# Optimization experiments

Measured on AMD Instinct MI355X. Metric: run time of the kernel, lower is better.

Reference implementation:

```python
import jax, jax.numpy as jnp
import numpy as np

B, T, D, NH, L, E, K = 2, 1024, 512, 8, 4, 8, 2
H = D * 4
HD = D // NH
EPS = 1e-5
THETA = 10000.0
MOE_LAYERS = (0, 2)   # layer_idx % moe_freq == 0
DENSE_LAYERS = (1, 3)


def setup_inputs() -> dict:
    key = jax.random.key(0)
    ks = jax.random.split(key, 12)
    s = 0.02
    return {
        "x": jax.random.normal(ks[0], (B, T, D), jnp.float32),
        "qkv_w": jax.random.normal(ks[1], (L, 3 * D, D), jnp.float32) * s,
        "out_w": jax.random.normal(ks[2], (L, D, D), jnp.float32) * s,
        "norm1_w": jnp.ones((L, D), jnp.float32),
        "norm2_w": jnp.ones((L, D), jnp.float32),
        "router_w": jax.random.normal(ks[3], (2, E, D), jnp.float32) * s,
        "moe_w1": jax.random.normal(ks[4], (2, E, H, D), jnp.float32) * s,
        "moe_w2": jax.random.normal(ks[5], (2, E, D, H), jnp.float32) * s,
        "moe_w3": jax.random.normal(ks[6], (2, E, H, D), jnp.float32) * s,
        "f_w1": jax.random.normal(ks[7], (2, H, D), jnp.float32) * s,
        "f_w2": jax.random.normal(ks[8], (2, D, H), jnp.float32) * s,
        "f_w3": jax.random.normal(ks[9], (2, H, D), jnp.float32) * s,
        "norm_f": jnp.ones((D,), jnp.float32),
    }


def rmsnorm(x, w):
    return w * x * jax.lax.rsqrt(jnp.mean(x * x, axis=-1, keepdims=True) + EPS)


def rope_tables():
    inv_freq = 1.0 / (THETA ** (jnp.arange(0, HD, 2, dtype=jnp.float32) / HD))  # [HD/2]
    t = jnp.arange(T, dtype=jnp.float32)
    freqs = t[:, None] * inv_freq[None, :]  # [T, HD/2]
    return jnp.cos(freqs), jnp.sin(freqs)


def apply_rope(x, cos, sin):  # x: [B, NH, T, HD]
    x1, x2 = jnp.split(x, 2, axis=-1)
    return jnp.concatenate([x1 * cos - x2 * sin, x1 * sin + x2 * cos], axis=-1)


def attention(x, qkv_w, out_w, cos, sin, causal):
    qkv = x @ qkv_w.T  # [B, T, 3D]
    q, k, v = jnp.split(qkv, 3, axis=-1)
    sh = lambda a: a.reshape(B, T, NH, HD).transpose(0, 2, 1, 3)  # [B, NH, T, HD]
    q, k, v = sh(q), sh(k), sh(v)
    q = apply_rope(q, cos, sin)
    k = apply_rope(k, cos, sin)
    scores = jnp.einsum('bhqd,bhkd->bhqk', q, k) / np.sqrt(HD).astype(np.float32)
    scores = jnp.where(causal, scores, jnp.finfo(scores.dtype).min)
    attn = jax.nn.softmax(scores, axis=-1)
    out = jnp.einsum('bhqk,bhkd->bhqd', attn, v)
    out = out.transpose(0, 2, 1, 3).reshape(B, T, D)
    return out @ out_w.T


def swiglu(x, w1, w2, w3):
    return (jax.nn.silu(x @ w1.T) * (x @ w3.T)) @ w2.T


def moe(x, rw, w1, w2, w3):  # x: [N, D]
    n = x.shape[0]
    logits = x @ rw.T                              # [N, E]
    top_v, top_i = jax.lax.top_k(logits, K)        # [N, K]
    wts = jax.nn.softmax(top_v, axis=-1)           # [N, K]
    # combine[t, e] = sum_i wts[t, i] * 1[top_i[t, i] == e]
    combine = jnp.zeros((n, E), x.dtype).at[jnp.arange(n)[:, None], top_i].add(wts)
    gate = jax.nn.silu(jnp.einsum('nd,ehd->neh', x, w1))
    up = jnp.einsum('nd,ehd->neh', x, w3)
    expert_out = jnp.einsum('neh,edh->ned', gate * up, w2)  # [N, E, D]
    return jnp.einsum('ne,ned->nd', combine, expert_out)


def reference(x, qkv_w, out_w, norm1_w, norm2_w, router_w, moe_w1, moe_w2,
              moe_w3, f_w1, f_w2, f_w3, norm_f):
    cos, sin = rope_tables()
    causal = jnp.tril(jnp.ones((T, T), bool))
    h = x
    for l in range(L):
        h = h + attention(rmsnorm(h, norm1_w[l]), qkv_w[l], out_w[l], cos, sin, causal)
        hn = rmsnorm(h, norm2_w[l])
        if l in MOE_LAYERS:
            m = MOE_LAYERS.index(l)
            ff = moe(hn.reshape(-1, D), router_w[m], moe_w1[m], moe_w2[m], moe_w3[m]).reshape(B, T, D)
        else:
            m = DENSE_LAYERS.index(l)
            ff = swiglu(hn, f_w1[m], f_w2[m], f_w3[m])
        h = h + ff
    return rmsnorm(h, norm_f)
```

## Files before the change

kernel.cpp:

```cpp
#include <hip/hip_runtime.h>
#include <hip/hip_bf16.h>
#include <math.h>

#define Bc 2
#define Tc 1024
#define Dc 512
#define NHc 8
#define Lc 4
#define Ec 8
#define Kc 2
#define Hc 2048
#define HDc 64
#define Nc (Bc * Tc)
#define NKc (Nc * Kc)

typedef __bf16 bf16x8 __attribute__((ext_vector_type(8)));
typedef float  f32x4  __attribute__((ext_vector_type(4)));
typedef unsigned short ushort8v __attribute__((ext_vector_type(8)));
typedef unsigned short ushort4v __attribute__((ext_vector_type(4)));

__device__ inline unsigned short f2bf(float f) {
    union { float f; unsigned u; } v; v.f = f;
    unsigned r = v.u + 0x7FFFu + ((v.u >> 16) & 1u);
    return (unsigned short)(r >> 16);
}
__device__ inline float bf2f(unsigned short b) {
    union { unsigned u; float f; } v; v.u = ((unsigned)b) << 16;
    return v.f;
}
__device__ inline void splitbf(float a, unsigned short& hi, unsigned short& lo) {
    unsigned short h = f2bf(a);
    hi = h;
    lo = f2bf(a - bf2f(h));
}

__global__ __launch_bounds__(256) void split_w_kernel(
    const float* __restrict__ w, unsigned short* __restrict__ hi,
    unsigned short* __restrict__ lo, int n4)
{
    int i = blockIdx.x * 256 + threadIdx.x;
    if (i >= n4) return;
    float4 v = ((const float4*)w)[i];
    ushort4v h, l;
    unsigned short a, b;
    splitbf(v.x, a, b); h[0] = a; l[0] = b;
    splitbf(v.y, a, b); h[1] = a; l[1] = b;
    splitbf(v.z, a, b); h[2] = a; l[2] = b;
    splitbf(v.w, a, b); h[3] = a; l[3] = b;
    ((ushort4v*)hi)[i] = h;
    ((ushort4v*)lo)[i] = l;
}

__global__ __launch_bounds__(256) void rmsnorm_split_kernel(
    const float* __restrict__ x, const float* __restrict__ w,
    float* __restrict__ y, unsigned short* __restrict__ yh,
    unsigned short* __restrict__ yl)
{
    int row = blockIdx.x;
    const float* xr = x + (size_t)row * Dc;
    __shared__ float red[256];
    int tid = threadIdx.x;
    float ss = 0.0f;
    for (int d = tid; d < Dc; d += 256) { float v = xr[d]; ss += v * v; }
    red[tid] = ss; __syncthreads();
    for (int s = 128; s > 0; s >>= 1) {
        if (tid < s) red[tid] += red[tid + s];
        __syncthreads();
    }
    float inv = rsqrtf(red[0] / (float)Dc + 1e-5f);
    for (int d = tid; d < Dc; d += 256) {
        float v = w[d] * xr[d] * inv;
        size_t idx = (size_t)row * Dc + d;
        y[idx] = v;
        unsigned short h, l;
        splitbf(v, h, l);
        yh[idx] = h; yl[idx] = l;
    }
}

__global__ __launch_bounds__(256) void rmsnorm_kernel(
    const float* __restrict__ x, const float* __restrict__ w,
    float* __restrict__ y)
{
    int row = blockIdx.x;
    const float* xr = x + (size_t)row * Dc;
    __shared__ float red[256];
    int tid = threadIdx.x;
    float ss = 0.0f;
    for (int d = tid; d < Dc; d += 256) { float v = xr[d]; ss += v * v; }
    red[tid] = ss; __syncthreads();
    for (int s = 128; s > 0; s >>= 1) {
        if (tid < s) red[tid] += red[tid + s];
        __syncthreads();
    }
    float inv = rsqrtf(red[0] / (float)Dc + 1e-5f);
    for (int d = tid; d < Dc; d += 256)
        y[(size_t)row * Dc + d] = w[d] * xr[d] * inv;
}

template<int MODE, int TM, int TN, int KSPLIT>
__global__ __launch_bounds__(256) void gemm3p(
    const unsigned short* __restrict__ Ahi, const unsigned short* __restrict__ Alo,
    const unsigned short* __restrict__ Whibase, const unsigned short* __restrict__ Wlobase,
    float* __restrict__ C, int M, int N, int K,
    const int* __restrict__ tok, const float* __restrict__ twt,
    const int* __restrict__ counts, const int* __restrict__ offsets,
    size_t wstride)
{
    constexpr int PAD = 40;
    constexpr int PA  = TM / 64;
    constexpr int PB  = TN / 64;
    constexpr int FM  = TM / 32;
    constexpr int FN  = TN / 32;

    int zz = blockIdx.z;
    int e  = (MODE == 5) ? zz / KSPLIT : 0;
    int kz = (MODE == 5) ? zz % KSPLIT : zz;
    int count = M, offs = 0;
    if (MODE == 5) {
        count = counts[e];
        offs  = offsets[e];
        if ((int)(blockIdx.y * TM) >= count) return;
    }
    const unsigned short* Whi = Whibase + (size_t)e * wstride;
    const unsigned short* Wlo = Wlobase + (size_t)e * wstride;

    int Ksub = K / KSPLIT;
    int kbeg = kz * Ksub;

    __shared__ __align__(16) unsigned short Ah[TM][PAD];
    __shared__ __align__(16) unsigned short Al[TM][PAD];
    __shared__ __align__(16) unsigned short Bh[TN][PAD];
    __shared__ __align__(16) unsigned short Bl[TN][PAD];

    int tid = threadIdx.x;
    int m0 = blockIdx.y * TM, n0 = blockIdx.x * TN;
    int srow = tid >> 2;
    int scol = (tid & 3) * 8;

    int wave = tid >> 6, lane = tid & 63;
    int wm = wave >> 1, wn = wave & 1;
    int quad = lane >> 4, l16 = lane & 15;

    f32x4 acc[FM][FN];
#pragma unroll
    for (int mi = 0; mi < FM; ++mi)
#pragma unroll
        for (int ni = 0; ni < FN; ++ni)
            acc[mi][ni] = (f32x4){0.f, 0.f, 0.f, 0.f};

    size_t arow[PA];
#pragma unroll
    for (int p = 0; p < PA; ++p) {
        int row = p * 64 + srow;
        if (MODE == 5) {
            int rr = m0 + row; if (rr >= count) rr = 0;
            arow[p] = (size_t)(offs + rr) * K;
        } else {
            arow[p] = (size_t)(m0 + row) * K;
        }
    }
    size_t brow[PB];
#pragma unroll
    for (int p = 0; p < PB; ++p)
        brow[p] = (size_t)(n0 + p * 64 + srow) * K;

#define G3_LOAD(AH, AL, BH, BL, KN)                                       \
    {                                                                     \
        _Pragma("unroll")                                                 \
        for (int p = 0; p < PA; ++p) {                                    \
            AH[p] = *(const ushort8v*)(Ahi + arow[p] + (KN) + scol);      \
            AL[p] = *(const ushort8v*)(Alo + arow[p] + (KN) + scol);      \
        }                                                                 \
        _Pragma("unroll")                                                 \
        for (int p = 0; p < PB; ++p) {                                    \
            BH[p] = *(const ushort8v*)(Whi + brow[p] + (KN) + scol);      \
            BL[p] = *(const ushort8v*)(Wlo + brow[p] + (KN) + scol);      \
        }                                                                 \
    }

#define G3_STORE(AH, AL, BH, BL)                                          \
    {                                                                     \
        _Pragma("unroll")                                                 \
        for (int p = 0; p < PA; ++p) {                                    \
            *(ushort8v*)&Ah[p * 64 + srow][scol] = AH[p];                 \
            *(ushort8v*)&Al[p * 64 + srow][scol] = AL[p];                 \
        }                                                                 \
        _Pragma("unroll")                                                 \
        for (int p = 0; p < PB; ++p) {                                    \
            *(ushort8v*)&Bh[p * 64 + srow][scol] = BH[p];                 \
            *(ushort8v*)&Bl[p * 64 + srow][scol] = BL[p];                 \
        }                                                                 \
    }

#define G3_COMPUTE()                                                      \
    {                                                                     \
        bf16x8 ah[FM], al[FM], bh[FN], bl[FN];                            \
        _Pragma("unroll")                                                 \
        for (int mi = 0; mi < FM; ++mi) {                                 \
            ah[mi] = *(const bf16x8*)&Ah[wm * (TM / 2) + mi * 16 + l16][quad * 8]; \
            al[mi] = *(const bf16x8*)&Al[wm * (TM / 2) + mi * 16 + l16][quad * 8]; \
        }                                                                 \
        _Pragma("unroll")                                                 \
        for (int ni = 0; ni < FN; ++ni) {                                 \
            bh[ni] = *(const bf16x8*)&Bh[wn * (TN / 2) + ni * 16 + l16][quad * 8]; \
            bl[ni] = *(const bf16x8*)&Bl[wn * (TN / 2) + ni * 16 + l16][quad * 8]; \
        }                                                                 \
        _Pragma("unroll")                                                 \
        for (int mi = 0; mi < FM; ++mi)                                   \
            _Pragma("unroll")                                             \
            for (int ni = 0; ni < FN; ++ni) {                             \
                acc[mi][ni] = __builtin_amdgcn_mfma_f32_16x16x32_bf16(    \
                    ah[mi], bh[ni], acc[mi][ni], 0, 0, 0);                \
                acc[mi][ni] = __builtin_amdgcn_mfma_f32_16x16x32_bf16(    \
                    al[mi], bh[ni], acc[mi][ni], 0, 0, 0);                \
                acc[mi][ni] = __builtin_amdgcn_mfma_f32_16x16x32_bf16(    \
                    ah[mi], bl[ni], acc[mi][ni], 0, 0, 0);                \
            }                                                             \
    }

    ushort8v a0h[PA], a0l[PA], b0h[PB], b0l[PB];
    ushort8v a1h[PA], a1l[PA], b1h[PB], b1l[PB];
    G3_LOAD(a0h, a0l, b0h, b0l, kbeg)
    G3_LOAD(a1h, a1l, b1h, b1l, kbeg + 32)

    for (int k0 = kbeg; k0 < kbeg + Ksub; k0 += 64) {
        G3_STORE(a0h, a0l, b0h, b0l)
        __syncthreads();
        if (k0 + 64 < kbeg + Ksub) G3_LOAD(a0h, a0l, b0h, b0l, k0 + 64)
        G3_COMPUTE()
        __syncthreads();
        G3_STORE(a1h, a1l, b1h, b1l)
        __syncthreads();
        if (k0 + 96 < kbeg + Ksub) G3_LOAD(a1h, a1l, b1h, b1l, k0 + 96)
        G3_COMPUTE()
        __syncthreads();
    }
#undef G3_LOAD
#undef G3_STORE
#undef G3_COMPUTE

#pragma unroll
    for (int mi = 0; mi < FM; ++mi) {
#pragma unroll
        for (int ni = 0; ni < FN; ++ni) {
            int col = n0 + wn * (TN / 2) + ni * 16 + l16;
#pragma unroll
            for (int r = 0; r < 4; ++r) {
                int row = wm * (TM / 2) + mi * 16 + quad * 4 + r;
                float v = acc[mi][ni][r];
                if (MODE == 0) {
                    C[(size_t)(m0 + row) * N + col] = v;
                } else if (MODE == 1) {
                    C[(size_t)(m0 + row) * N + col] += v;
                } else if (MODE == 2) {
                    atomicAdd(&C[(size_t)(m0 + row) * N + col], v);
                } else {
                    int rr = m0 + row;
                    if (rr < count) {
                        int dest = tok[offs + rr];
                        float w = twt[offs + rr];
                        atomicAdd(&C[(size_t)dest * N + col], w * v);
                    }
                }
            }
        }
    }
}

template<bool GATHER>
__global__ __launch_bounds__(512) void ffn_fusedp(
    const unsigned short* __restrict__ Ahi, const unsigned short* __restrict__ Alo,
    const unsigned short* __restrict__ W1hibase, const unsigned short* __restrict__ W1lobase,
    const unsigned short* __restrict__ W3hibase, const unsigned short* __restrict__ W3lobase,
    unsigned short* __restrict__ Thi, unsigned short* __restrict__ Tlo,
    int M, int N, int K,
    const int* __restrict__ tok, const int* __restrict__ counts,
    const int* __restrict__ offsets, size_t wstride)
{
    constexpr int TM = 128, TN = 128, PAD = 40;
    constexpr int FM = 4, FN = 2;

    int e = GATHER ? blockIdx.z : 0;
    int count = M, offs = 0;
    if (GATHER) {
        count = counts[e];
        offs  = offsets[e];
        if ((int)(blockIdx.y * TM) >= count) return;
    }
    const unsigned short* W1hi = W1hibase + (size_t)e * wstride;
    const unsigned short* W1lo = W1lobase + (size_t)e * wstride;
    const unsigned short* W3hi = W3hibase + (size_t)e * wstride;
    const unsigned short* W3lo = W3lobase + (size_t)e * wstride;

    __shared__ __align__(16) unsigned short Ah[TM][PAD];
    __shared__ __align__(16) unsigned short Al[TM][PAD];
    __shared__ __align__(16) unsigned short B1h[TN][PAD];
    __shared__ __align__(16) unsigned short B1l[TN][PAD];
    __shared__ __align__(16) unsigned short B3h[TN][PAD];
    __shared__ __align__(16) unsigned short B3l[TN][PAD];
    __shared__ int sTok[TM];

    int tid = threadIdx.x;
    int m0 = blockIdx.y * TM, n0 = blockIdx.x * TN;

    if (GATHER) {
        if (tid < TM) {
            int r = m0 + tid;
            sTok[tid] = (r < count) ? tok[offs + r] : tok[offs];
        }
        __syncthreads();
    }

    int srow = tid >> 2;
    int scol = (tid & 3) * 8;
    int wave = tid >> 6, lane = tid & 63;
    int wm = wave >> 2, wn = wave & 3;
    int quad = lane >> 4, l16 = lane & 15;

    f32x4 accg[FM][FN], accu[FM][FN];
#pragma unroll
    for (int mi = 0; mi < FM; ++mi)
#pragma unroll
        for (int ni = 0; ni < FN; ++ni) {
            accg[mi][ni] = (f32x4){0.f, 0.f, 0.f, 0.f};
            accu[mi][ni] = (f32x4){0.f, 0.f, 0.f, 0.f};
        }

    size_t arow;
    if (GATHER) arow = (size_t)sTok[srow] * K;
    else        arow = (size_t)(m0 + srow) * K;
    size_t brow = (size_t)(n0 + srow) * K;

    ushort8v pah, pal, p1h, p1l, p3h, p3l;
    pah = *(const ushort8v*)(Ahi + arow + scol);
    pal = *(const ushort8v*)(Alo + arow + scol);
    p1h = *(const ushort8v*)(W1hi + brow + scol);
    p1l = *(const ushort8v*)(W1lo + brow + scol);
    p3h = *(const ushort8v*)(W3hi + brow + scol);
    p3l = *(const ushort8v*)(W3lo + brow + scol);

    for (int k0 = 0; k0 < K; k0 += 32) {
        *(ushort8v*)&Ah[srow][scol]  = pah;
        *(ushort8v*)&Al[srow][scol]  = pal;
        *(ushort8v*)&B1h[srow][scol] = p1h;
        *(ushort8v*)&B1l[srow][scol] = p1l;
        *(ushort8v*)&B3h[srow][scol] = p3h;
        *(ushort8v*)&B3l[srow][scol] = p3l;
        __syncthreads();
        if (k0 + 32 < K) {
            int kn = k0 + 32;
            pah = *(const ushort8v*)(Ahi + arow + kn + scol);
            pal = *(const ushort8v*)(Alo + arow + kn + scol);
            p1h = *(const ushort8v*)(W1hi + brow + kn + scol);
            p1l = *(const ushort8v*)(W1lo + brow + kn + scol);
            p3h = *(const ushort8v*)(W3hi + brow + kn + scol);
            p3l = *(const ushort8v*)(W3lo + brow + kn + scol);
        }

        bf16x8 ah[FM], al[FM];
#pragma unroll
        for (int mi = 0; mi < FM; ++mi) {
            ah[mi] = *(const bf16x8*)&Ah[wm * 64 + mi * 16 + l16][quad * 8];
            al[mi] = *(const bf16x8*)&Al[wm * 64 + mi * 16 + l16][quad * 8];
        }
        {
            bf16x8 bh[FN], bl[FN];
#pragma unroll
            for (int ni = 0; ni < FN; ++ni) {
                bh[ni] = *(const bf16x8*)&B1h[wn * 32 + ni * 16 + l16][quad * 8];
                bl[ni] = *(const bf16x8*)&B1l[wn * 32 + ni * 16 + l16][quad * 8];
            }
#pragma unroll
            for (int mi = 0; mi < FM; ++mi)
#pragma unroll
                for (int ni = 0; ni < FN; ++ni) {
                    accg[mi][ni] = __builtin_amdgcn_mfma_f32_16x16x32_bf16(
                        ah[mi], bh[ni], accg[mi][ni], 0, 0, 0);
                    accg[mi][ni] = __builtin_amdgcn_mfma_f32_16x16x32_bf16(
                        al[mi], bh[ni], accg[mi][ni], 0, 0, 0);
                    accg[mi][ni] = __builtin_amdgcn_mfma_f32_16x16x32_bf16(
                        ah[mi], bl[ni], accg[mi][ni], 0, 0, 0);
                }
        }
        {
            bf16x8 bh[FN], bl[FN];
#pragma unroll
            for (int ni = 0; ni < FN; ++ni) {
                bh[ni] = *(const bf16x8*)&B3h[wn * 32 + ni * 16 + l16][quad * 8];
                bl[ni] = *(const bf16x8*)&B3l[wn * 32 + ni * 16 + l16][quad * 8];
            }
#pragma unroll
            for (int mi = 0; mi < FM; ++mi)
#pragma unroll
                for (int ni = 0; ni < FN; ++ni) {
                    accu[mi][ni] = __builtin_amdgcn_mfma_f32_16x16x32_bf16(
                        ah[mi], bh[ni], accu[mi][ni], 0, 0, 0);
                    accu[mi][ni] = __builtin_amdgcn_mfma_f32_16x16x32_bf16(
                        al[mi], bh[ni], accu[mi][ni], 0, 0, 0);
                    accu[mi][ni] = __builtin_amdgcn_mfma_f32_16x16x32_bf16(
                        ah[mi], bl[ni], accu[mi][ni], 0, 0, 0);
                }
        }
        __syncthreads();
    }

#pragma unroll
    for (int mi = 0; mi < FM; ++mi) {
#pragma unroll
        for (int ni = 0; ni < FN; ++ni) {
            int col = n0 + wn * 32 + ni * 16 + l16;
#pragma unroll
            for (int r = 0; r < 4; ++r) {
                int row = wm * 64 + mi * 16 + quad * 4 + r;
                float g = accg[mi][ni][r];
                float u = accu[mi][ni][r];
                float t = (g / (1.0f + expf(-g))) * u;
                unsigned short th, tl;
                splitbf(t, th, tl);
                if (GATHER) {
                    int rr = m0 + row;
                    if (rr < count) {
                        size_t idx = (size_t)(offs + rr) * N + col;
                        Thi[idx] = th; Tlo[idx] = tl;
                    }
                } else {
                    size_t idx = (size_t)(m0 + row) * N + col;
                    Thi[idx] = th; Tlo[idx] = tl;
                }
            }
        }
    }
}

__global__ __launch_bounds__(256) void rope_kernel(float* __restrict__ qkv)
{
    const int HD2 = HDc / 2;
    int idx = blockIdx.x * blockDim.x + threadIdx.x;
    int total = Nc * NHc * HD2;
    if (idx >= total) return;
    int i = idx % HD2;
    int hh = (idx / HD2) % NHc;
    int n = idx / (HD2 * NHc);
    int t = n % Tc;
    float invf = expf(-(2.0f * (float)i / (float)HDc) * logf(10000.0f));
    float f = (float)t * invf;
    float c = cosf(f), s = sinf(f);
    size_t base = (size_t)n * (3 * Dc) + (size_t)hh * HDc;
    float* qp = qkv + base;
    float* kp = qkv + base + Dc;
    float q1 = qp[i], q2 = qp[i + HD2];
    qp[i]       = q1 * c - q2 * s;
    qp[i + HD2] = q1 * s + q2 * c;
    float k1 = kp[i], k2 = kp[i + HD2];
    kp[i]       = k1 * c - k2 * s;
    kp[i + HD2] = k1 * s + k2 * c;
}

__global__ __launch_bounds__(256) void attn_mfma(
    const float* __restrict__ qkv, unsigned short* __restrict__ outh,
    unsigned short* __restrict__ outl)
{
    constexpr int PAD = 72;
    __shared__ __align__(16) unsigned short Qh[64][PAD];
    __shared__ __align__(16) unsigned short Ql[64][PAD];
    __shared__ __align__(16) unsigned short Kh[64][PAD];
    __shared__ __align__(16) unsigned short Kl[64][PAD];
    __shared__ __align__(16) unsigned short Vth[64][PAD];
    __shared__ __align__(16) unsigned short Vtl[64][PAD];

    int qb = blockIdx.x, bh = blockIdx.y;
    int b = bh >> 3, hh = bh & 7;
    const int D3 = 3 * Dc;
    const float* base = qkv + (size_t)b * Tc * D3 + (size_t)hh * HDc;

    int tid = threadIdx.x;
    int wave = tid >> 6, lane = tid & 63;
    int quad = lane >> 4, l16 = lane & 15;

    int srow = tid >> 2;
    int scb  = (tid & 3) * 16;
    int vhd  = lane;
    int vkb  = wave * 16;

    {
        const float* qp = base + (size_t)(qb * 64 + srow) * D3 + scb;
        float4 q0 = *(const float4*)(qp);
        float4 q1 = *(const float4*)(qp + 4);
        float4 q2 = *(const float4*)(qp + 8);
        float4 q3 = *(const float4*)(qp + 12);
        const float sc = 0.125f;
        q0.x *= sc; q0.y *= sc; q0.z *= sc; q0.w *= sc;
        q1.x *= sc; q1.y *= sc; q1.z *= sc; q1.w *= sc;
        q2.x *= sc; q2.y *= sc; q2.z *= sc; q2.w *= sc;
        q3.x *= sc; q3.y *= sc; q3.z *= sc; q3.w *= sc;
        unsigned short h, l;
        ushort8v hv, lv;
        splitbf(q0.x, h, l); hv[0] = h; lv[0] = l;
        splitbf(q0.y, h, l); hv[1] = h; lv[1] = l;
        splitbf(q0.z, h, l); hv[2] = h; lv[2] = l;
        splitbf(q0.w, h, l); hv[3] = h; lv[3] = l;
        splitbf(q1.x, h, l); hv[4] = h; lv[4] = l;
        splitbf(q1.y, h, l); hv[5] = h; lv[5] = l;
        splitbf(q1.z, h, l); hv[6] = h; lv[6] = l;
        splitbf(q1.w, h, l); hv[7] = h; lv[7] = l;
        *(ushort8v*)&Qh[srow][scb]     = hv;
        *(ushort8v*)&Ql[srow][scb]     = lv;
        splitbf(q2.x, h, l); hv[0] = h; lv[0] = l;
        splitbf(q2.y, h, l); hv[1] = h; lv[1] = l;
        splitbf(q2.z, h, l); hv[2] = h; lv[2] = l;
        splitbf(q2.w, h, l); hv[3] = h; lv[3] = l;
        splitbf(q3.x, h, l); hv[4] = h; lv[4] = l;
        splitbf(q3.y, h, l); hv[5] = h; lv[5] = l;
        splitbf(q3.z, h, l); hv[6] = h; lv[6] = l;
        splitbf(q3.w, h, l); hv[7] = h; lv[7] = l;
        *(ushort8v*)&Qh[srow][scb + 8] = hv;
        *(ushort8v*)&Ql[srow][scb + 8] = lv;
    }
    __syncthreads();
    bf16x8 qah[2], qal[2];
#pragma unroll
    for (int ks = 0; ks < 2; ++ks) {
        qah[ks] = *(const bf16x8*)&Qh[wave * 16 + l16][ks * 32 + quad * 8];
        qal[ks] = *(const bf16x8*)&Ql[wave * 16 + l16][ks * 32 + quad * 8];
    }

    float4 kf0, kf1, kf2, kf3;
    float vf[16];
    {
        const float* kp = base + (size_t)srow * D3 + Dc + scb;
        kf0 = *(const float4*)(kp);
        kf1 = *(const float4*)(kp + 4);
        kf2 = *(const float4*)(kp + 8);
        kf3 = *(const float4*)(kp + 12);
        const float* vp = base + (size_t)vkb * D3 + 2 * Dc + vhd;
#pragma unroll
        for (int i = 0; i < 16; ++i) vf[i] = vp[(size_t)i * D3];
    }

    f32x4 o[4];
#pragma unroll
    for (int f = 0; f < 4; ++f) o[f] = (f32x4){0.f, 0.f, 0.f, 0.f};
    float mrow[4], lrow[4];
#pragma unroll
    for (int r = 0; r < 4; ++r) { mrow[r] = -1e30f; lrow[r] = 0.0f; }

    for (int kt = 0; kt <= qb; ++kt) {
        __syncthreads();
        {
            unsigned short h, l;
            ushort8v hv, lv;
            splitbf(kf0.x, h, l); hv[0] = h; lv[0] = l;
            splitbf(kf0.y, h, l); hv[1] = h; lv[1] = l;
            splitbf(kf0.z, h, l); hv[2] = h; lv[2] = l;
            splitbf(kf0.w, h, l); hv[3] = h; lv[3] = l;
            splitbf(kf1.x, h, l); hv[4] = h; lv[4] = l;
            splitbf(kf1.y, h, l); hv[5] = h; lv[5] = l;
            splitbf(kf1.z, h, l); hv[6] = h; lv[6] = l;
            splitbf(kf1.w, h, l); hv[7] = h; lv[7] = l;
            *(ushort8v*)&Kh[srow][scb]     = hv;
            *(ushort8v*)&Kl[srow][scb]     = lv;
            splitbf(kf2.x, h, l); hv[0] = h; lv[0] = l;
            splitbf(kf2.y, h, l); hv[1] = h; lv[1] = l;
            splitbf(kf2.z, h, l); hv[2] = h; lv[2] = l;
            splitbf(kf2.w, h, l); hv[3] = h; lv[3] = l;
            splitbf(kf3.x, h, l); hv[4] = h; lv[4] = l;
            splitbf(kf3.y, h, l); hv[5] = h; lv[5] = l;
            splitbf(kf3.z, h, l); hv[6] = h; lv[6] = l;
            splitbf(kf3.w, h, l); hv[7] = h; lv[7] = l;
            *(ushort8v*)&Kh[srow][scb + 8] = hv;
            *(ushort8v*)&Kl[srow][scb + 8] = lv;
        }
        {
            unsigned short h, l;
            ushort8v hv, lv;
#pragma unroll
            for (int i = 0; i < 8; ++i) {
                splitbf(vf[i], h, l); hv[i] = h; lv[i] = l;
            }
            *(ushort8v*)&Vth[vhd][vkb]     = hv;
            *(ushort8v*)&Vtl[vhd][vkb]     = lv;
#pragma unroll
            for (int i = 0; i < 8; ++i) {
                splitbf(vf[8 + i], h, l); hv[i] = h; lv[i] = l;
            }
            *(ushort8v*)&Vth[vhd][vkb + 8] = hv;
            *(ushort8v*)&Vtl[vhd][vkb + 8] = lv;
        }
        __syncthreads();
        if (kt < qb) {
            const float* kp = base + (size_t)((kt + 1) * 64 + srow) * D3 + Dc + scb;
            kf0 = *(const float4*)(kp);
            kf1 = *(const float4*)(kp + 4);
            kf2 = *(const float4*)(kp + 8);
            kf3 = *(const float4*)(kp + 12);
            const float* vp = base + (size_t)((kt + 1) * 64 + vkb) * D3 + 2 * Dc + vhd;
#pragma unroll
            for (int i = 0; i < 16; ++i) vf[i] = vp[(size_t)i * D3];
        }

        f32x4 s[4];
#pragma unroll
        for (int ni = 0; ni < 4; ++ni) s[ni] = (f32x4){0.f, 0.f, 0.f, 0.f};
#pragma unroll
        for (int ks = 0; ks < 2; ++ks) {
            bf16x8 kh_[4], kl_[4];
#pragma unroll
            for (int ni = 0; ni < 4; ++ni) {
                kh_[ni] = *(const bf16x8*)&Kh[ni * 16 + l16][ks * 32 + quad * 8];
                kl_[ni] = *(const bf16x8*)&Kl[ni * 16 + l16][ks * 32 + quad * 8];
            }
#pragma unroll
            for (int ni = 0; ni < 4; ++ni) {
                s[ni] = __builtin_amdgcn_mfma_f32_16x16x32_bf16(
                    qah[ks], kh_[ni], s[ni], 0, 0, 0);
                s[ni] = __builtin_amdgcn_mfma_f32_16x16x32_bf16(
                    qal[ks], kh_[ni], s[ni], 0, 0, 0);
                s[ni] = __builtin_amdgcn_mfma_f32_16x16x32_bf16(
                    qah[ks], kl_[ni], s[ni], 0, 0, 0);
            }
        }

        if (kt == qb) {
#pragma unroll
            for (int ni = 0; ni < 4; ++ni)
#pragma unroll
                for (int r = 0; r < 4; ++r)
                    if (ni * 16 + l16 > wave * 16 + quad * 4 + r)
                        s[ni][r] = -1e30f;
        }

        float al4[4];
#pragma unroll
        for (int r = 0; r < 4; ++r) {
            float rm = fmaxf(fmaxf(s[0][r], s[1][r]), fmaxf(s[2][r], s[3][r]));
            rm = fmaxf(rm, __shfl_xor(rm, 1));
            rm = fmaxf(rm, __shfl_xor(rm, 2));
            rm = fmaxf(rm, __shfl_xor(rm, 4));
            rm = fmaxf(rm, __shfl_xor(rm, 8));
            float mn = fmaxf(mrow[r], rm);
            al4[r] = __expf(mrow[r] - mn);
            mrow[r] = mn;
            float rs = 0.0f;
#pragma unroll
            for (int ni = 0; ni < 4; ++ni) {
                float pv = __expf(s[ni][r] - mn);
                s[ni][r] = pv;
                rs += pv;
            }
            rs += __shfl_xor(rs, 1);
            rs += __shfl_xor(rs, 2);
            rs += __shfl_xor(rs, 4);
            rs += __shfl_xor(rs, 8);
            lrow[r] = lrow[r] * al4[r] + rs;
        }

        __syncthreads();
#pragma unroll
        for (int ni = 0; ni < 4; ++ni)
#pragma unroll
            for (int r = 0; r < 4; ++r) {
                unsigned short hp, lp;
                splitbf(s[ni][r], hp, lp);
                Kh[wave * 16 + quad * 4 + r][ni * 16 + l16] = hp;
                Kl[wave * 16 + quad * 4 + r][ni * 16 + l16] = lp;
            }
#pragma unroll
        for (int f = 0; f < 4; ++f)
#pragma unroll
            for (int r = 0; r < 4; ++r)
                o[f][r] *= al4[r];
#pragma unroll
        for (int ks = 0; ks < 2; ++ks) {
            bf16x8 pah = *(const bf16x8*)&Kh[wave * 16 + l16][ks * 32 + quad * 8];
            bf16x8 pal = *(const bf16x8*)&Kl[wave * 16 + l16][ks * 32 + quad * 8];
#pragma unroll
            for (int f = 0; f < 4; ++f) {
                bf16x8 vh_ = *(const bf16x8*)&Vth[f * 16 + l16][ks * 32 + quad * 8];
                bf16x8 vl_ = *(const bf16x8*)&Vtl[f * 16 + l16][ks * 32 + quad * 8];
                o[f] = __builtin_amdgcn_mfma_f32_16x16x32_bf16(
                    pah, vh_, o[f], 0, 0, 0);
                o[f] = __builtin_amdgcn_mfma_f32_16x16x32_bf16(
                    pal, vh_, o[f], 0, 0, 0);
                o[f] = __builtin_amdgcn_mfma_f32_16x16x32_bf16(
                    pah, vl_, o[f], 0, 0, 0);
            }
        }
    }

#pragma unroll
    for (int r = 0; r < 4; ++r) {
        float inv = 1.0f / lrow[r];
        int q = qb * 64 + wave * 16 + quad * 4 + r;
#pragma unroll
        for (int f = 0; f < 4; ++f) {
            size_t idx = (size_t)(b * Tc + q) * Dc + hh * HDc + f * 16 + l16;
            unsigned short hp, lp;
            splitbf(o[f][r] * inv, hp, lp);
            outh[idx] = hp; outl[idx] = lp;
        }
    }
}

__global__ __launch_bounds__(64) void router_kernel(
    const float* __restrict__ x, const float* __restrict__ rw,
    float* __restrict__ logits)
{
    int n = blockIdx.x;
    int lane = threadIdx.x;
    const float* xr = x + (size_t)n * Dc;
    for (int e = 0; e < Ec; ++e) {
        const float* wr = rw + (size_t)e * Dc;
        float p = 0.0f;
        for (int d = lane; d < Dc; d += 64) p += xr[d] * wr[d];
        for (int off = 32; off > 0; off >>= 1) p += __shfl_down(p, off);
        if (lane == 0) logits[(size_t)n * Ec + e] = p;
    }
}

__global__ void zero8_kernel(int* __restrict__ counts)
{
    if (threadIdx.x < Ec) counts[threadIdx.x] = 0;
}

__global__ __launch_bounds__(256) void topk_count_kernel(
    const float* __restrict__ logits, int* __restrict__ counts,
    int2* __restrict__ eidx, float2* __restrict__ ewt)
{
    int n = blockIdx.x * blockDim.x + threadIdx.x;
    if (n >= Nc) return;
    const float* lg = logits + (size_t)n * Ec;
    int i0 = -1, i1 = -1;
    float v0 = -1e30f, v1 = -1e30f;
    for (int e = 0; e < Ec; ++e) {
        float v = lg[e];
        if (v > v0) { v1 = v0; i1 = i0; v0 = v; i0 = e; }
        else if (v > v1) { v1 = v; i1 = e; }
    }
    float e1 = expf(v1 - v0);
    float w0 = 1.0f / (1.0f + e1);
    float w1 = e1 / (1.0f + e1);
    atomicAdd(&counts[i0], 1);
    atomicAdd(&counts[i1], 1);
    eidx[n] = make_int2(i0, i1);
    ewt[n]  = make_float2(w0, w1);
}

__global__ void scan_kernel(int* __restrict__ counts, int* __restrict__ offsets)
{
    if (threadIdx.x == 0) {
        int s = 0;
        for (int e = 0; e < Ec; ++e) { offsets[e] = s; s += counts[e]; counts[e] = 0; }
    }
}

__global__ __launch_bounds__(256) void topk_place_kernel(
    const int2* __restrict__ eidx, const float2* __restrict__ ewt,
    int* __restrict__ counts, const int* __restrict__ offsets,
    int* __restrict__ tok, float* __restrict__ twt)
{
    int n = blockIdx.x * blockDim.x + threadIdx.x;
    if (n >= Nc) return;
    int2 ei = eidx[n];
    float2 w = ewt[n];
    int p0 = atomicAdd(&counts[ei.x], 1);
    int r0 = offsets[ei.x] + p0;
    tok[r0] = n; twt[r0] = w.x;
    int p1 = atomicAdd(&counts[ei.y], 1);
    int r1 = offsets[ei.y] + p1;
    tok[r1] = n; twt[r1] = w.y;
}

extern "C" void kernel_launch(void* const* d_in, const int* in_sizes, int n_in,
                              void* d_out, int out_size, void* d_ws, size_t ws_size,
                              hipStream_t stream)
{
    const float* x        = (const float*)d_in[0];
    const float* qkv_w    = (const float*)d_in[1];
    const float* out_w    = (const float*)d_in[2];
    const float* norm1_w  = (const float*)d_in[3];
    const float* norm2_w  = (const float*)d_in[4];
    const float* router_w = (const float*)d_in[5];
    const float* moe_w1   = (const float*)d_in[6];
    const float* moe_w2   = (const float*)d_in[7];
    const float* moe_w3   = (const float*)d_in[8];
    const float* f_w1     = (const float*)d_in[9];
    const float* f_w2     = (const float*)d_in[10];
    const float* f_w3     = (const float*)d_in[11];
    const float* norm_f   = (const float*)d_in[12];
    float* out = (float*)d_out;

    float* p = (float*)d_ws;
    float* h      = p;  p += Nc * Dc;
    float* xn     = p;  p += Nc * Dc;
    unsigned short* xnh = (unsigned short*)p;  p += Nc * Dc / 2;
    unsigned short* xnl = (unsigned short*)p;  p += Nc * Dc / 2;
    float* arena  = p;  p += (size_t)NKc * Hc;
    float* logits = p;  p += Nc * Ec;
    int*   counts  = (int*)p;  p += 16;
    int*   offsets = (int*)p;  p += 16;
    int2*  eidx    = (int2*)p; p += 2 * Nc;
    float* ewt     = p;        p += 2 * Nc;
    int*   tok     = (int*)p;  p += NKc;
    float* twt     = p;        p += NKc;
    unsigned short* wqh = (unsigned short*)p;
    unsigned short* wql = wqh + (size_t)3 * Dc * Dc;
    unsigned short* woh = wql + (size_t)3 * Dc * Dc;
    unsigned short* wol = woh + (size_t)Dc * Dc;
    unsigned short* wah = wol + (size_t)Dc * Dc;
    unsigned short* wal = wah + (size_t)Ec * Hc * Dc;
    unsigned short* wbh = wal + (size_t)Ec * Hc * Dc;
    unsigned short* wbl = wbh + (size_t)Ec * Hc * Dc;

    float* qkv = arena;
    unsigned short* th = (unsigned short*)arena;
    unsigned short* tl = th + (size_t)NKc * Hc;

    hipMemcpyAsync(h, x, (size_t)Nc * Dc * sizeof(float),
                   hipMemcpyDeviceToDevice, stream);

    for (int l = 0; l < Lc; ++l) {
        {
            int n4 = 3 * Dc * Dc / 4;
            split_w_kernel<<<(n4 + 255) / 256, 256, 0, stream>>>(
                qkv_w + (size_t)l * 3 * Dc * Dc, wqh, wql, n4);
        }
        rmsnorm_split_kernel<<<Nc, 256, 0, stream>>>(
            h, norm1_w + (size_t)l * Dc, xn, xnh, xnl);
        gemm3p<0, 64, 128, 1><<<dim3(3 * Dc / 128, Nc / 64, 1), 256, 0, stream>>>(
            xnh, xnl, wqh, wql, qkv, Nc, 3 * Dc, Dc,
            nullptr, nullptr, nullptr, nullptr, 0);
        {
            int total = Nc * NHc * (HDc / 2);
            rope_kernel<<<(total + 255) / 256, 256, 0, stream>>>(qkv);
        }
        {
            int n4 = Dc * Dc / 4;
            split_w_kernel<<<(n4 + 255) / 256, 256, 0, stream>>>(
                out_w + (size_t)l * Dc * Dc, woh, wol, n4);
        }
        attn_mfma<<<dim3(Tc / 64, Bc * NHc), 256, 0, stream>>>(qkv, xnh, xnl);
        gemm3p<2, 64, 64, 2><<<dim3(Dc / 64, Nc / 64, 2), 256, 0, stream>>>(
            xnh, xnl, woh, wol, h, Nc, Dc, Dc,
            nullptr, nullptr, nullptr, nullptr, 0);

        rmsnorm_split_kernel<<<Nc, 256, 0, stream>>>(
            h, norm2_w + (size_t)l * Dc, xn, xnh, xnl);
        if (l == 0 || l == 2) {
            int m = l / 2;
            router_kernel<<<Nc, 64, 0, stream>>>(
                xn, router_w + (size_t)m * Ec * Dc, logits);
            zero8_kernel<<<1, 64, 0, stream>>>(counts);
            topk_count_kernel<<<Nc / 256, 256, 0, stream>>>(
                logits, counts, eidx, (float2*)ewt);
            scan_kernel<<<1, 64, 0, stream>>>(counts, offsets);
            topk_place_kernel<<<Nc / 256, 256, 0, stream>>>(
                eidx, (float2*)ewt, counts, offsets, tok, twt);

            int n4 = Ec * Hc * Dc / 4;
            split_w_kernel<<<(n4 + 255) / 256, 256, 0, stream>>>(
                moe_w1 + (size_t)m * Ec * Hc * Dc, wah, wal, n4);
            split_w_kernel<<<(n4 + 255) / 256, 256, 0, stream>>>(
                moe_w3 + (size_t)m * Ec * Hc * Dc, wbh, wbl, n4);
            ffn_fusedp<true><<<dim3(Hc / 128, NKc / 128, Ec), 512, 0, stream>>>(
                xnh, xnl, wah, wal, wbh, wbl, th, tl, Nc, Hc, Dc,
                tok, counts, offsets, (size_t)Hc * Dc);
            split_w_kernel<<<(n4 + 255) / 256, 256, 0, stream>>>(
                moe_w2 + (size_t)m * Ec * Dc * Hc, wah, wal, n4);
            gemm3p<5, 64, 128, 2><<<dim3(Dc / 128, NKc / 64, Ec * 2), 256, 0, stream>>>(
                th, tl, wah, wal, h, Nc, Dc, Hc,
                tok, twt, counts, offsets, (size_t)Dc * Hc);
        } else {
            int m = (l - 1) / 2;
            int n4 = Hc * Dc / 4;
            split_w_kernel<<<(n4 + 255) / 256, 256, 0, stream>>>(
                f_w1 + (size_t)m * Hc * Dc, wah, wal, n4);
            split_w_kernel<<<(n4 + 255) / 256, 256, 0, stream>>>(
                f_w3 + (size_t)m * Hc * Dc, wbh, wbl, n4);
            ffn_fusedp<false><<<dim3(Hc / 128, Nc / 128, 1), 512, 0, stream>>>(
                xnh, xnl, wah, wal, wbh, wbl, th, tl, Nc, Hc, Dc,
                nullptr, nullptr, nullptr, 0);
            split_w_kernel<<<(n4 + 255) / 256, 256, 0, stream>>>(
                f_w2 + (size_t)m * Dc * Hc, wah, wal, n4);
            gemm3p<2, 64, 128, 2><<<dim3(Dc / 128, Nc / 64, 2), 256, 0, stream>>>(
                th, tl, wah, wal, h, Nc, Dc, Hc,
                nullptr, nullptr, nullptr, nullptr, 0);
        }
    }

    rmsnorm_kernel<<<Nc, 256, 0, stream>>>(h, norm_f, out);
}
```

Before: 1.244 ms.

## Remap GEMM block indices across XCDs and deepen FFN register prefetch

```diff
diff --git a/kernel.cpp b/kernel.cpp
--- a/kernel.cpp
+++ b/kernel.cpp
@@ -34,6 +34,17 @@
     lo = f2bf(a - bf2f(h));
 }
 
+__device__ inline void xcd_remap_bmajor(int& bx, int& by) {
+    int gx = gridDim.x, gy = gridDim.y;
+    int p = by * gx + bx;
+    int total = gx * gy;
+    int q = total >> 3, r = total & 7;
+    int xcd = p & 7, slot = p >> 3;
+    int L = (xcd < r ? xcd * (q + 1) : r * (q + 1) + (xcd - r) * q) + slot;
+    bx = L / gy;
+    by = L % gy;
+}
+
 __global__ __launch_bounds__(256) void split_w_kernel(
     const float* __restrict__ w, unsigned short* __restrict__ hi,
     unsigned short* __restrict__ lo, int n4)
@@ -120,10 +131,13 @@
     if (MODE == 5) {
         count = counts[e];
         offs  = offsets[e];
-        if ((int)(blockIdx.y * TM) >= count) return;
     }
     const unsigned short* Whi = Whibase + (size_t)e * wstride;
     const unsigned short* Wlo = Wlobase + (size_t)e * wstride;
+
+    int bx = blockIdx.x, by = blockIdx.y;
+    xcd_remap_bmajor(bx, by);
+    if (MODE == 5 && by * TM >= count) return;
 
     int Ksub = K / KSPLIT;
     int kbeg = kz * Ksub;
@@ -134,7 +148,7 @@
     __shared__ __align__(16) unsigned short Bl[TN][PAD];
 
     int tid = threadIdx.x;
-    int m0 = blockIdx.y * TM, n0 = blockIdx.x * TN;
+    int m0 = by * TM, n0 = bx * TN;
     int srow = tid >> 2;
     int scol = (tid & 3) * 8;
 
@@ -286,12 +300,15 @@
     if (GATHER) {
         count = counts[e];
         offs  = offsets[e];
-        if ((int)(blockIdx.y * TM) >= count) return;
     }
     const unsigned short* W1hi = W1hibase + (size_t)e * wstride;
     const unsigned short* W1lo = W1lobase + (size_t)e * wstride;
     const unsigned short* W3hi = W3hibase + (size_t)e * wstride;
     const unsigned short* W3lo = W3lobase + (size_t)e * wstride;
+
+    int bx = blockIdx.x, by = blockIdx.y;
+    xcd_remap_bmajor(bx, by);
+    if (GATHER && by * TM >= count) return;
 
     __shared__ __align__(16) unsigned short Ah[TM][PAD];
     __shared__ __align__(16) unsigned short Al[TM][PAD];
@@ -302,7 +319,7 @@
     __shared__ int sTok[TM];
 
     int tid = threadIdx.x;
-    int m0 = blockIdx.y * TM, n0 = blockIdx.x * TN;
+    int m0 = by * TM, n0 = bx * TN;
 
     if (GATHER) {
         if (tid < TM) {
@@ -332,78 +349,94 @@
     else        arow = (size_t)(m0 + srow) * K;
     size_t brow = (size_t)(n0 + srow) * K;
 
-    ushort8v pah, pal, p1h, p1l, p3h, p3l;
-    pah = *(const ushort8v*)(Ahi + arow + scol);
-    pal = *(const ushort8v*)(Alo + arow + scol);
-    p1h = *(const ushort8v*)(W1hi + brow + scol);
-    p1l = *(const ushort8v*)(W1lo + brow + scol);
-    p3h = *(const ushort8v*)(W3hi + brow + scol);
-    p3l = *(const ushort8v*)(W3lo + brow + scol);
-
-    for (int k0 = 0; k0 < K; k0 += 32) {
-        *(ushort8v*)&Ah[srow][scol]  = pah;
-        *(ushort8v*)&Al[srow][scol]  = pal;
-        *(ushort8v*)&B1h[srow][scol] = p1h;
-        *(ushort8v*)&B1l[srow][scol] = p1l;
-        *(ushort8v*)&B3h[srow][scol] = p3h;
-        *(ushort8v*)&B3l[srow][scol] = p3l;
-        __syncthreads();
-        if (k0 + 32 < K) {
-            int kn = k0 + 32;
-            pah = *(const ushort8v*)(Ahi + arow + kn + scol);
-            pal = *(const ushort8v*)(Alo + arow + kn + scol);
-            p1h = *(const ushort8v*)(W1hi + brow + kn + scol);
-            p1l = *(const ushort8v*)(W1lo + brow + kn + scol);
-            p3h = *(const ushort8v*)(W3hi + brow + kn + scol);
-            p3l = *(const ushort8v*)(W3lo + brow + kn + scol);
-        }
-
-        bf16x8 ah[FM], al[FM];
-#pragma unroll
-        for (int mi = 0; mi < FM; ++mi) {
-            ah[mi] = *(const bf16x8*)&Ah[wm * 64 + mi * 16 + l16][quad * 8];
-            al[mi] = *(const bf16x8*)&Al[wm * 64 + mi * 16 + l16][quad * 8];
-        }
-        {
-            bf16x8 bh[FN], bl[FN];
-#pragma unroll
-            for (int ni = 0; ni < FN; ++ni) {
-                bh[ni] = *(const bf16x8*)&B1h[wn * 32 + ni * 16 + l16][quad * 8];
-                bl[ni] = *(const bf16x8*)&B1l[wn * 32 + ni * 16 + l16][quad * 8];
-            }
-#pragma unroll
-            for (int mi = 0; mi < FM; ++mi)
-#pragma unroll
-                for (int ni = 0; ni < FN; ++ni) {
-                    accg[mi][ni] = __builtin_amdgcn_mfma_f32_16x16x32_bf16(
-                        ah[mi], bh[ni], accg[mi][ni], 0, 0, 0);
-                    accg[mi][ni] = __builtin_amdgcn_mfma_f32_16x16x32_bf16(
-                        al[mi], bh[ni], accg[mi][ni], 0, 0, 0);
-                    accg[mi][ni] = __builtin_amdgcn_mfma_f32_16x16x32_bf16(
-                        ah[mi], bl[ni], accg[mi][ni], 0, 0, 0);
-                }
-        }
-        {
-            bf16x8 bh[FN], bl[FN];
-#pragma unroll
-            for (int ni = 0; ni < FN; ++ni) {
-                bh[ni] = *(const bf16x8*)&B3h[wn * 32 + ni * 16 + l16][quad * 8];
-                bl[ni] = *(const bf16x8*)&B3l[wn * 32 + ni * 16 + l16][quad * 8];
-            }
-#pragma unroll
-            for (int mi = 0; mi < FM; ++mi)
-#pragma unroll
-                for (int ni = 0; ni < FN; ++ni) {
-                    accu[mi][ni] = __builtin_amdgcn_mfma_f32_16x16x32_bf16(
-                        ah[mi], bh[ni], accu[mi][ni], 0, 0, 0);
-                    accu[mi][ni] = __builtin_amdgcn_mfma_f32_16x16x32_bf16(
-                        al[mi], bh[ni], accu[mi][ni], 0, 0, 0);
-                    accu[mi][ni] = __builtin_amdgcn_mfma_f32_16x16x32_bf16(
-                        ah[mi], bl[ni], accu[mi][ni], 0, 0, 0);
-                }
-        }
-        __syncthreads();
-    }
+#define FF_LOAD(AH, AL, B1H, B1L, B3H, B3L, KN)                           \
+    {                                                                     \
+        AH  = *(const ushort8v*)(Ahi  + arow + (KN) + scol);              \
+        AL  = *(const ushort8v*)(Alo  + arow + (KN) + scol);              \
+        B1H = *(const ushort8v*)(W1hi + brow + (KN) + scol);              \
+        B1L = *(const ushort8v*)(W1lo + brow + (KN) + scol);              \
+        B3H = *(const ushort8v*)(W3hi + brow + (KN) + scol);              \
+        B3L = *(const ushort8v*)(W3lo + brow + (KN) + scol);              \
+    }
+
+#define FF_STORE(AH, AL, B1H, B1L, B3H, B3L)                              \
+    {                                                                     \
+        *(ushort8v*)&Ah[srow][scol]  = AH;                                \
+        *(ushort8v*)&Al[srow][scol]  = AL;                                \
+        *(ushort8v*)&B1h[srow][scol] = B1H;                               \
+        *(ushort8v*)&B1l[srow][scol] = B1L;                               \
+        *(ushort8v*)&B3h[srow][scol] = B3H;                               \
+        *(ushort8v*)&B3l[srow][scol] = B3L;                               \
+    }
+
+#define FF_COMPUTE()                                                      \
+    {                                                                     \
+        bf16x8 ah[FM], al[FM];                                            \
+        _Pragma("unroll")                                                 \
+        for (int mi = 0; mi < FM; ++mi) {                                 \
+            ah[mi] = *(const bf16x8*)&Ah[wm * 64 + mi * 16 + l16][quad * 8]; \
+            al[mi] = *(const bf16x8*)&Al[wm * 64 + mi * 16 + l16][quad * 8]; \
+        }                                                                 \
+        {                                                                 \
+            bf16x8 bh[FN], bl[FN];                                        \
+            _Pragma("unroll")                                             \
+            for (int ni = 0; ni < FN; ++ni) {                             \
+                bh[ni] = *(const bf16x8*)&B1h[wn * 32 + ni * 16 + l16][quad * 8]; \
+                bl[ni] = *(const bf16x8*)&B1l[wn * 32 + ni * 16 + l16][quad * 8]; \
+            }                                                             \
+            _Pragma("unroll")                                             \
+            for (int mi = 0; mi < FM; ++mi)                               \
+                _Pragma("unroll")                                         \
+                for (int ni = 0; ni < FN; ++ni) {                         \
+                    accg[mi][ni] = __builtin_amdgcn_mfma_f32_16x16x32_bf16( \
+                        ah[mi], bh[ni], accg[mi][ni], 0, 0, 0);           \
+                    accg[mi][ni] = __builtin_amdgcn_mfma_f32_16x16x32_bf16( \
+                        al[mi], bh[ni], accg[mi][ni], 0, 0, 0);           \
+                    accg[mi][ni] = __builtin_amdgcn_mfma_f32_16x16x32_bf16( \
+                        ah[mi], bl[ni], accg[mi][ni], 0, 0, 0);           \
+                }                                                         \
+        }                                                                 \
+        {                                                                 \
+            bf16x8 bh[FN], bl[FN];                                        \
+            _Pragma("unroll")                                             \
+            for (int ni = 0; ni < FN; ++ni) {                             \
+                bh[ni] = *(const bf16x8*)&B3h[wn * 32 + ni * 16 + l16][quad * 8]; \
+                bl[ni] = *(const bf16x8*)&B3l[wn * 32 + ni * 16 + l16][quad * 8]; \
+            }                                                             \
+            _Pragma("unroll")                                             \
+            for (int mi = 0; mi < FM; ++mi)                               \
+                _Pragma("unroll")                                         \
+                for (int ni = 0; ni < FN; ++ni) {                         \
+                    accu[mi][ni] = __builtin_amdgcn_mfma_f32_16x16x32_bf16( \
+                        ah[mi], bh[ni], accu[mi][ni], 0, 0, 0);           \
+                    accu[mi][ni] = __builtin_amdgcn_mfma_f32_16x16x32_bf16( \
+                        al[mi], bh[ni], accu[mi][ni], 0, 0, 0);           \
+                    accu[mi][ni] = __builtin_amdgcn_mfma_f32_16x16x32_bf16( \
+                        ah[mi], bl[ni], accu[mi][ni], 0, 0, 0);           \
+                }                                                         \
+        }                                                                 \
+    }
+
+    ushort8v s0a, s0al, s0b1, s0b1l, s0b3, s0b3l;
+    ushort8v s1a, s1al, s1b1, s1b1l, s1b3, s1b3l;
+    FF_LOAD(s0a, s0al, s0b1, s0b1l, s0b3, s0b3l, 0)
+    FF_LOAD(s1a, s1al, s1b1, s1b1l, s1b3, s1b3l, 32)
+
+    for (int k0 = 0; k0 < K; k0 += 64) {
+        FF_STORE(s0a, s0al, s0b1, s0b1l, s0b3, s0b3l)
+        __syncthreads();
+        if (k0 + 64 < K) FF_LOAD(s0a, s0al, s0b1, s0b1l, s0b3, s0b3l, k0 + 64)
+        FF_COMPUTE()
+        __syncthreads();
+        FF_STORE(s1a, s1al, s1b1, s1b1l, s1b3, s1b3l)
+        __syncthreads();
+        if (k0 + 96 < K) FF_LOAD(s1a, s1al, s1b1, s1b1l, s1b3, s1b3l, k0 + 96)
+        FF_COMPUTE()
+        __syncthreads();
+    }
+#undef FF_LOAD
+#undef FF_STORE
+#undef FF_COMPUTE
 
 #pragma unroll
     for (int mi = 0; mi < FM; ++mi) {
```

New measurement: 1.336 ms. 1.07x slower.
